# Optimization experiments

Hardware: AMD Instinct MI355X
Metric: run time of the kernel (lower is better)

Reference implementation:

```python
import jax, jax.numpy as jnp
import numpy as np

N_NODES = 50000
N_EDGES = 800000
IN_FEAT = 256
OUT_FEAT = 256
NUM_RELS = 8
ALPHA = 0.5


def setup_inputs() -> dict:
    key = jax.random.key(0)
    k1, k2, k3, k4, k5, k6 = jax.random.split(key, 6)
    x = jax.random.normal(k1, (N_NODES, IN_FEAT), dtype=jnp.float32)
    edge_index = jax.random.randint(k2, (2, N_EDGES), 0, N_NODES, dtype=jnp.int64)
    edge_type = jax.random.randint(k3, (N_EDGES,), 0, NUM_RELS, dtype=jnp.int64)
    # Xavier-uniform-ish init for weights (scale per fan-in/fan-out)
    gain = float(np.sqrt(2.0))  # calculate_gain('relu')
    lim_w = gain * float(np.sqrt(6.0 / (IN_FEAT + OUT_FEAT)))
    weight = jax.random.uniform(k4, (NUM_RELS, IN_FEAT, OUT_FEAT), dtype=jnp.float32,
                                minval=-lim_w, maxval=lim_w)
    loop_weight = jax.random.uniform(k5, (IN_FEAT, OUT_FEAT), dtype=jnp.float32,
                                     minval=-lim_w, maxval=lim_w)
    h_bias = jnp.zeros((OUT_FEAT,), dtype=jnp.float32)
    return {"edge_index": edge_index, "x": x, "edge_type": edge_type,
            "weight": weight, "h_bias": h_bias, "loop_weight": loop_weight}


def reference(edge_index, x, edge_type, weight, h_bias, loop_weight):
    num_nodes = x.shape[0]
    src, dst = edge_index[0], edge_index[1]
    # Per-edge message msg_e = x[src_e] @ weight[edge_type_e].
    # Computed efficiently as num_rels dense GEMMs over all nodes, then a fused
    # (relation, src) gather — identical math, avoids (E, in, out) weight blowup.
    hx = jnp.einsum('ni,rio->rno', x, weight)          # (R, N, out)
    msg = hx[edge_type, src]                            # (E, out)
    agg = jax.ops.segment_sum(msg, dst, num_segments=num_nodes)  # (N, out)
    node_repr = agg * jnp.asarray(ALPHA, x.dtype) ** 0.5
    node_repr = node_repr + h_bias
    loop_message = x @ loop_weight                      # (N, out)
    node_repr = node_repr + loop_message * jnp.asarray(1.0 - ALPHA, x.dtype) ** 0.5
    # activation=None, dropout=0.0 (eval) -> identity
    return node_repr
```

## Files before the change

kernel.cpp:

```cpp
#include <hip/hip_runtime.h>

typedef __bf16 bf16x8 __attribute__((ext_vector_type(8)));
typedef float f32x4 __attribute__((ext_vector_type(4)));

static __device__ __forceinline__ unsigned short f2bf(float f) {
    unsigned u = __builtin_bit_cast(unsigned, f);
    u += 0x7FFFu + ((u >> 16) & 1u);
    return (unsigned short)(u >> 16);
}
static __device__ __forceinline__ float bf2f(unsigned short h) {
    return __builtin_bit_cast(float, ((unsigned)h) << 16);
}

#define GLOAD_LDS16(g, l)                                              \
    __builtin_amdgcn_global_load_lds(                                  \
        (const __attribute__((address_space(1))) unsigned int*)(g),    \
        (__attribute__((address_space(3))) unsigned int*)(l), 16, 0, 0)

__global__ __launch_bounds__(256) void rgcn_prep(const int* __restrict__ ei,
                                                 unsigned* __restrict__ cnt,
                                                 const float* __restrict__ x,
                                                 unsigned short* __restrict__ Z,
                                                 const float* __restrict__ w,
                                                 const float* __restrict__ lw,
                                                 unsigned short* __restrict__ wbT,
                                                 int E, int M, int HB, int CB) {
    const int b = blockIdx.x;
    const int t = threadIdx.x;
    if (b < HB) {
        int e = b * 256 + t;
        if (e < E) atomicAdd(&cnt[ei[E + e]], 1u);
    } else if (b < HB + CB) {
        int wv = ((b - HB) * 256 + t) >> 6;
        int lane = t & 63;
        if (wv < M) {
            float4 v = *(const float4*)(x + (size_t)wv * 256 + lane * 4);
            ushort4 o;
            o.x = f2bf(v.x); o.y = f2bf(v.y); o.z = f2bf(v.z); o.w = f2bf(v.w);
            *(ushort4*)(Z + (size_t)wv * 2304 + 2048 + lane * 4) = o;
        }
    } else {
        int bb = b - HB - CB;
        int kc = (bb % 9) * 256 + t;
        int n  = bb / 9;
        if (kc < 2304) {
            float v;
            if (kc < 2048) {
                int r = kc >> 8, k = kc & 255;
                v = w[((size_t)r * 256 + k) * 256 + n];
            } else {
                v = lw[(size_t)(kc - 2048) * 256 + n];
            }
            wbT[(size_t)n * 2304 + kc] = f2bf(v * 0.70710678118654752f);
        }
    }
}

__global__ __launch_bounds__(1024) void rgcn_scan_all(const unsigned* __restrict__ cnt,
                                                      unsigned* __restrict__ off,
                                                      unsigned* __restrict__ cur,
                                                      unsigned* __restrict__ done,
                                                      unsigned* __restrict__ bsum,
                                                      int n, int nb) {
    __shared__ unsigned wsum[16];
    __shared__ unsigned bpre_s;
    const int t = threadIdx.x, lane = t & 63, wv = t >> 6;
    const int b = blockIdx.x;
    int i = b * 1024 + t;
    unsigned v = (i < n) ? cnt[i] : 0;
    unsigned s = v;
    #pragma unroll
    for (int d = 1; d < 64; d <<= 1) {
        unsigned u = __shfl_up(s, d, 64);
        if (lane >= d) s += u;
    }
    if (lane == 63) wsum[wv] = s;
    __syncthreads();
    if (wv == 0) {
        unsigned bb = (lane < 16) ? wsum[lane] : 0;
        unsigned sb = bb;
        #pragma unroll
        for (int d = 1; d < 16; d <<= 1) {
            unsigned u = __shfl_up(sb, d, 64);
            if (lane >= d) sb += u;
        }
        if (lane < 16) wsum[lane] = sb - bb;
        if (lane == 15) {
            atomicExch(&bsum[b], sb);
            __threadfence();
            atomicAdd(done, 1u);
        }
    }
    __syncthreads();
    if (t == 0) {
        while (atomicAdd(done, 0u) < (unsigned)nb) __builtin_amdgcn_s_sleep(8);
    }
    __syncthreads();
    if (wv == 0) {
        unsigned bv = (lane < nb) ? atomicAdd(&bsum[lane], 0u) : 0;
        unsigned sp = bv;
        #pragma unroll
        for (int d = 1; d < 64; d <<= 1) {
            unsigned u = __shfl_up(sp, d, 64);
            if (lane >= d) sp += u;
        }
        if (lane == b) bpre_s = sp - bv;
        if (b == 0 && lane == nb - 1) off[n] = sp;
    }
    __syncthreads();
    unsigned base = bpre_s + wsum[wv];
    if (i < n) {
        unsigned o = base + (s - v);
        off[i] = o;
        cur[i] = o;
    }
}

__global__ __launch_bounds__(256) void rgcn_scatter(const int* __restrict__ ei,
                                                    const int* __restrict__ et,
                                                    unsigned* __restrict__ cur,
                                                    unsigned* __restrict__ recs, int E) {
    int e = blockIdx.x * 256 + threadIdx.x;
    if (e < E) {
        int dst = ei[E + e];
        unsigned p = atomicAdd(&cur[dst], 1u);
        recs[p] = (unsigned)ei[e] | ((unsigned)et[e] << 16);
    }
}

__global__ __launch_bounds__(256) void rgcn_agg(const unsigned* __restrict__ recs,
                                                const unsigned* __restrict__ off,
                                                unsigned short* __restrict__ Z, int M) {
    const int gw0  = (blockIdx.x * 256 + threadIdx.x) >> 6;
    const int nw   = (gridDim.x * 256) >> 6;
    const int lane = threadIdx.x & 63;
    const unsigned short* Zx = Z + 2048 + lane * 4;

#define GATHER(rr) (*(const ushort4*)(Zx + (size_t)((rr) & 0xFFFFu) * 2304))
#define ACCUM(rec, v_)                                                                 \
    {                                                                                  \
        f32x4 fv;                                                                      \
        fv[0] = bf2f(v_.x); fv[1] = bf2f(v_.y); fv[2] = bf2f(v_.z); fv[3] = bf2f(v_.w);\
        switch ((rec) >> 16) {                                                         \
            case 0: a0 += fv; break; case 1: a1 += fv; break;                          \
            case 2: a2 += fv; break; case 3: a3 += fv; break;                          \
            case 4: a4 += fv; break; case 5: a5 += fv; break;                          \
            case 6: a6 += fv; break; default: a7 += fv; break;                         \
        }                                                                              \
    }

    for (int w = gw0; w < M; w += nw) {
        const unsigned o0 = off[w], o1 = off[w + 1];
        f32x4 a0 = {}, a1 = {}, a2 = {}, a3 = {}, a4 = {}, a5 = {}, a6 = {}, a7 = {};

        for (unsigned base = o0; base < o1; base += 64) {
            const unsigned wdeg = (o1 - base < 64u) ? (o1 - base) : 64u;
            const unsigned myrec = ((unsigned)lane < wdeg) ? recs[base + lane] : 0u;

            unsigned j = 0;
            for (; j + 16 <= wdeg; j += 16) {
                unsigned rr[16];
                #pragma unroll
                for (int u = 0; u < 16; ++u) rr[u] = __shfl(myrec, (int)(j + u), 64);
                ushort4 vv[16];
                #pragma unroll
                for (int u = 0; u < 16; ++u) vv[u] = GATHER(rr[u]);
                #pragma unroll
                for (int u = 0; u < 16; ++u) ACCUM(rr[u], vv[u]);
            }
            for (; j + 4 <= wdeg; j += 4) {
                unsigned rr[4];
                #pragma unroll
                for (int u = 0; u < 4; ++u) rr[u] = __shfl(myrec, (int)(j + u), 64);
                ushort4 vv[4];
                #pragma unroll
                for (int u = 0; u < 4; ++u) vv[u] = GATHER(rr[u]);
                #pragma unroll
                for (int u = 0; u < 4; ++u) ACCUM(rr[u], vv[u]);
            }
            for (; j < wdeg; ++j) {
                unsigned r_ = __shfl(myrec, (int)j, 64);
                ushort4 v_ = GATHER(r_);
                ACCUM(r_, v_);
            }
        }

        unsigned short* zr = Z + (size_t)w * 2304 + lane * 4;
#define ST(rr_, ax)                                                                    \
        {                                                                              \
            ushort4 o_;                                                                \
            o_.x = f2bf(ax[0]); o_.y = f2bf(ax[1]);                                    \
            o_.z = f2bf(ax[2]); o_.w = f2bf(ax[3]);                                    \
            *(ushort4*)(zr + rr_ * 256) = o_;                                          \
        }
        ST(0, a0) ST(1, a1) ST(2, a2) ST(3, a3) ST(4, a4) ST(5, a5) ST(6, a6) ST(7, a7)
#undef ST
    }
#undef GATHER
#undef ACCUM
}

#define BM 256
#define BK 64
#define NCH 36

__global__ __launch_bounds__(512) void rgcn_gemm(
    const unsigned short* __restrict__ A,
    const unsigned short* __restrict__ Bt,
    float* __restrict__ out,
    const float* __restrict__ bias,
    int M)
{
    __shared__ char lds[4 * 32768];
    char* Ab0 = lds;
    char* Ab1 = lds + 32768;
    char* Bb0 = lds + 65536;
    char* Bb1 = lds + 98304;

    const int tid  = threadIdx.x;
    const int lane = tid & 63;
    const int wid  = tid >> 6;
    const int wm   = (wid >> 1) * 64;
    const int wn   = (wid & 1) * 128;
    const int m0   = blockIdx.x * BM;

    f32x4 acc[4][8] = {};

    auto stageA = [&](int chunk, char* dst) {
        #pragma unroll
        for (int it = 0; it < 4; ++it) {
            int o   = it * 8192 + tid * 16;
            int r   = o >> 7;
            int scb = (o & 127) ^ ((r & 7) << 4);
            int ga  = m0 + r; if (ga >= M) ga = M - 1;
            GLOAD_LDS16((const char*)A + (size_t)ga * 4608 + (size_t)chunk * 128 + scb, dst + o);
        }
    };
    auto stageB = [&](int chunk, char* dst) {
        #pragma unroll
        for (int it = 0; it < 4; ++it) {
            int o   = it * 8192 + tid * 16;
            int r   = o >> 7;
            int scb = (o & 127) ^ ((r & 7) << 4);
            GLOAD_LDS16((const char*)Bt + (size_t)r * 4608 + (size_t)chunk * 128 + scb, dst + o);
        }
    };

    stageA(0, Ab0); stageB(0, Bb0);
    stageA(1, Ab1); stageB(1, Bb1);
    asm volatile("s_waitcnt vmcnt(8)" ::: "memory");
    __builtin_amdgcn_s_barrier();
    __builtin_amdgcn_sched_barrier(0);

    for (int t = 0; t < NCH; ++t) {
        const char* Ac = (t & 1) ? Ab1 : Ab0;
        const char* Bc = (t & 1) ? Bb1 : Bb0;
        #pragma unroll
        for (int kk = 0; kk < 2; ++kk) {
            const int koff = kk * 32 + (lane >> 4) * 8;
            bf16x8 af[4], bfr[8];
            #pragma unroll
            for (int i = 0; i < 4; ++i) {
                int ar = wm + i * 16 + (lane & 15);
                af[i] = *(const bf16x8*)(Ac + ((ar * 128 + koff * 2) ^ ((ar & 7) << 4)));
            }
            #pragma unroll
            for (int j = 0; j < 8; ++j) {
                int br = wn + j * 16 + (lane & 15);
                bfr[j] = *(const bf16x8*)(Bc + ((br * 128 + koff * 2) ^ ((br & 7) << 4)));
            }
            #pragma unroll
            for (int i = 0; i < 4; ++i)
                #pragma unroll
                for (int j = 0; j < 8; ++j)
                    acc[i][j] = __builtin_amdgcn_mfma_f32_16x16x32_bf16(af[i], bfr[j], acc[i][j], 0, 0, 0);
        }

        if (t < NCH - 1) {
            __builtin_amdgcn_s_barrier();
            __builtin_amdgcn_sched_barrier(0);
            int tn = (t + 2 < NCH) ? t + 2 : NCH - 1;
            stageA(tn, (t & 1) ? Ab1 : Ab0);
            stageB(tn, (t & 1) ? Bb1 : Bb0);
            asm volatile("s_waitcnt vmcnt(8)" ::: "memory");
            __builtin_amdgcn_s_barrier();
            __builtin_amdgcn_sched_barrier(0);
        }
    }
    asm volatile("s_waitcnt vmcnt(0)" ::: "memory");

    const int col = lane & 15;
    const int r0  = (lane >> 4) * 4;
    #pragma unroll
    for (int i = 0; i < 4; ++i) {
        #pragma unroll
        for (int j = 0; j < 8; ++j) {
            int gn = wn + j * 16 + col;
            float bv = bias[gn];
            #pragma unroll
            for (int rr = 0; rr < 4; ++rr) {
                int gm = m0 + wm + i * 16 + r0 + rr;
                if (gm < M) out[(size_t)gm * 256 + gn] = acc[i][j][rr] + bv;
            }
        }
    }
}

extern "C" void kernel_launch(void* const* d_in, const int* in_sizes, int n_in,
                              void* d_out, int out_size, void* d_ws, size_t ws_size,
                              hipStream_t stream) {
    const int*   edge_index = (const int*)d_in[0];
    const float* x          = (const float*)d_in[1];
    const int*   edge_type  = (const int*)d_in[2];
    const float* weight     = (const float*)d_in[3];
    const float* h_bias     = (const float*)d_in[4];
    const float* loop_w     = (const float*)d_in[5];
    float* out = (float*)d_out;

    const int M = in_sizes[1] / 256;
    const int E = in_sizes[2];

    char* ws = (char*)d_ws;
    size_t off_b = 0;
    unsigned short* Zcat = (unsigned short*)(ws + off_b);
    off_b += (((size_t)M * 2304 * 2) + 255) & ~(size_t)255;
    unsigned short* wbT = (unsigned short*)(ws + off_b);
    off_b += (((size_t)256 * 2304 * 2) + 255) & ~(size_t)255;
    unsigned* cnt = (unsigned*)(ws + off_b);
    unsigned* done = cnt + M;
    unsigned* bsum = cnt + M + 2;
    off_b += (((size_t)(M + 2 + 64) * 4) + 255) & ~(size_t)255;
    unsigned* off = (unsigned*)(ws + off_b);
    off_b += (((size_t)(M + 1) * 4) + 255) & ~(size_t)255;
    unsigned* cur = (unsigned*)(ws + off_b);
    off_b += (((size_t)M * 4) + 255) & ~(size_t)255;
    unsigned* recs = (unsigned*)(ws + off_b);

    const int nb = (M + 1023) / 1024;
    const int HB = (E + 255) / 256;
    const int CB = (M + 3) / 4;

    (void)hipMemsetAsync(cnt, 0, (size_t)(M + 2 + 64) * 4, stream);

    rgcn_prep<<<HB + CB + 2304, 256, 0, stream>>>(edge_index, cnt, x, Zcat,
                                                  weight, loop_w, wbT, E, M, HB, CB);
    rgcn_scan_all<<<nb, 1024, 0, stream>>>(cnt, off, cur, done, bsum, M, nb);
    rgcn_scatter<<<(E + 255) / 256, 256, 0, stream>>>(edge_index, edge_type, cur, recs, E);

    rgcn_agg<<<2560, 256, 0, stream>>>(recs, off, Zcat, M);

    rgcn_gemm<<<(M + BM - 1) / BM, 512, 0, stream>>>(Zcat, wbT, out, h_bias, M);
}
```

Baseline: 311.5 us.

## Split aggregation into four column-slice passes for cache locality

The aggregation kernel now runs in four launches. Each launch handles a 64-column slice of the bf16 gathered features, with one scalar element per lane instead of four. The idea is that each pass's gathered working set (64 columns of x for all nodes) fits better in L2/MALL, so the random gathers hit cache more often. The cost is that record reads and shuffles happen four times, the gathers become 2-byte per lane (128 bytes per wave) instead of 8-byte, and outputs are written with nontemporal stores.

```diff
diff --git a/kernel.cpp b/kernel.cpp
--- a/kernel.cpp
+++ b/kernel.cpp
@@ -130,17 +130,17 @@
 
 __global__ __launch_bounds__(256) void rgcn_agg(const unsigned* __restrict__ recs,
                                                 const unsigned* __restrict__ off,
-                                                unsigned short* __restrict__ Z, int M) {
+                                                unsigned short* __restrict__ Z,
+                                                int M, int pass) {
     const int gw0  = (blockIdx.x * 256 + threadIdx.x) >> 6;
     const int nw   = (gridDim.x * 256) >> 6;
     const int lane = threadIdx.x & 63;
-    const unsigned short* Zx = Z + 2048 + lane * 4;
-
-#define GATHER(rr) (*(const ushort4*)(Zx + (size_t)((rr) & 0xFFFFu) * 2304))
+    const unsigned short* Zx = Z + 2048 + pass * 64 + lane;
+
+#define GATHER(rr) (Zx[(size_t)((rr) & 0xFFFFu) * 2304])
 #define ACCUM(rec, v_)                                                                 \
     {                                                                                  \
-        f32x4 fv;                                                                      \
-        fv[0] = bf2f(v_.x); fv[1] = bf2f(v_.y); fv[2] = bf2f(v_.z); fv[3] = bf2f(v_.w);\
+        float fv = bf2f(v_);                                                           \
         switch ((rec) >> 16) {                                                         \
             case 0: a0 += fv; break; case 1: a1 += fv; break;                          \
             case 2: a2 += fv; break; case 3: a3 += fv; break;                          \
@@ -151,7 +151,7 @@
 
     for (int w = gw0; w < M; w += nw) {
         const unsigned o0 = off[w], o1 = off[w + 1];
-        f32x4 a0 = {}, a1 = {}, a2 = {}, a3 = {}, a4 = {}, a5 = {}, a6 = {}, a7 = {};
+        float a0 = 0, a1 = 0, a2 = 0, a3 = 0, a4 = 0, a5 = 0, a6 = 0, a7 = 0;
 
         for (unsigned base = o0; base < o1; base += 64) {
             const unsigned wdeg = (o1 - base < 64u) ? (o1 - base) : 64u;
@@ -162,7 +162,7 @@
                 unsigned rr[16];
                 #pragma unroll
                 for (int u = 0; u < 16; ++u) rr[u] = __shfl(myrec, (int)(j + u), 64);
-                ushort4 vv[16];
+                unsigned short vv[16];
                 #pragma unroll
                 for (int u = 0; u < 16; ++u) vv[u] = GATHER(rr[u]);
                 #pragma unroll
@@ -172,7 +172,7 @@
                 unsigned rr[4];
                 #pragma unroll
                 for (int u = 0; u < 4; ++u) rr[u] = __shfl(myrec, (int)(j + u), 64);
-                ushort4 vv[4];
+                unsigned short vv[4];
                 #pragma unroll
                 for (int u = 0; u < 4; ++u) vv[u] = GATHER(rr[u]);
                 #pragma unroll
@@ -180,21 +180,20 @@
             }
             for (; j < wdeg; ++j) {
                 unsigned r_ = __shfl(myrec, (int)j, 64);
-                ushort4 v_ = GATHER(r_);
+                unsigned short v_ = GATHER(r_);
                 ACCUM(r_, v_);
             }
         }
 
-        unsigned short* zr = Z + (size_t)w * 2304 + lane * 4;
-#define ST(rr_, ax)                                                                    \
-        {                                                                              \
-            ushort4 o_;                                                                \
-            o_.x = f2bf(ax[0]); o_.y = f2bf(ax[1]);                                    \
-            o_.z = f2bf(ax[2]); o_.w = f2bf(ax[3]);                                    \
-            *(ushort4*)(zr + rr_ * 256) = o_;                                          \
-        }
-        ST(0, a0) ST(1, a1) ST(2, a2) ST(3, a3) ST(4, a4) ST(5, a5) ST(6, a6) ST(7, a7)
-#undef ST
+        unsigned short* zr = Z + (size_t)w * 2304 + pass * 64 + lane;
+        __builtin_nontemporal_store(f2bf(a0), zr);
+        __builtin_nontemporal_store(f2bf(a1), zr + 256);
+        __builtin_nontemporal_store(f2bf(a2), zr + 512);
+        __builtin_nontemporal_store(f2bf(a3), zr + 768);
+        __builtin_nontemporal_store(f2bf(a4), zr + 1024);
+        __builtin_nontemporal_store(f2bf(a5), zr + 1280);
+        __builtin_nontemporal_store(f2bf(a6), zr + 1536);
+        __builtin_nontemporal_store(f2bf(a7), zr + 1792);
     }
 #undef GATHER
 #undef ACCUM
@@ -347,7 +346,10 @@
     rgcn_scan_all<<<nb, 1024, 0, stream>>>(cnt, off, cur, done, bsum, M, nb);
     rgcn_scatter<<<(E + 255) / 256, 256, 0, stream>>>(edge_index, edge_type, cur, recs, E);
 
-    rgcn_agg<<<2560, 256, 0, stream>>>(recs, off, Zcat, M);
+    rgcn_agg<<<2560, 256, 0, stream>>>(recs, off, Zcat, M, 0);
+    rgcn_agg<<<2560, 256, 0, stream>>>(recs, off, Zcat, M, 1);
+    rgcn_agg<<<2560, 256, 0, stream>>>(recs, off, Zcat, M, 2);
+    rgcn_agg<<<2560, 256, 0, stream>>>(recs, off, Zcat, M, 3);
 
     rgcn_gemm<<<(M + BM - 1) / BM, 512, 0, stream>>>(Zcat, wbT, out, h_bias, M);
 }
```

New measurement: 458.4 us. +47.2%, slower.
